# Performance work log

Hardware: AMD Instinct MI355X
Metric: run time of the kernel (lower is better)

## Reference

```python
import jax, jax.numpy as jnp
import numpy as np

B, T, D = 4, 2048, 1024
EPS = 1e-5


def _layernorm(x, g, b):
    mu = jnp.mean(x, axis=-1, keepdims=True)
    var = jnp.var(x, axis=-1, keepdims=True)
    return (x - mu) * jax.lax.rsqrt(var + EPS) * g + b


def setup_inputs() -> dict:
    key = jax.random.key(0)
    ks = jax.random.split(key, 16)
    s = lambda fan_in: 1.0 / np.sqrt(fan_in)
    return {
        "x": jax.random.normal(ks[0], (B, T, D), dtype=jnp.float32),
        "ln1_g": jnp.ones((D,), jnp.float32),
        "ln1_b": jnp.zeros((D,), jnp.float32),
        "Wqkv": jax.random.uniform(ks[1], (D, 3 * D), jnp.float32, -s(D), s(D)),
        "bqkv": jnp.zeros((3 * D,), jnp.float32),
        "Wproj": jax.random.uniform(ks[2], (D, D), jnp.float32, -s(D), s(D)),
        "bproj": jnp.zeros((D,), jnp.float32),
        "ln2_g": jnp.ones((D,), jnp.float32),
        "ln2_b": jnp.zeros((D,), jnp.float32),
        "W1": jax.random.uniform(ks[3], (D, 4 * D), jnp.float32, -s(D), s(D)),
        "b1": jnp.zeros((4 * D,), jnp.float32),
        "W2": jax.random.uniform(ks[4], (4 * D, D), jnp.float32, -s(4 * D), s(4 * D)),
        "b2": jnp.zeros((D,), jnp.float32),
    }


def reference(x, ln1_g, ln1_b, Wqkv, bqkv, Wproj, bproj, ln2_g, ln2_b, W1, b1, W2, b2):
    # NOTE: no residual connections in the original Block.
    h = _layernorm(x, ln1_g, ln1_b)
    kqv = h @ Wqkv + bqkv                      # [B,T,3D]
    k, q, v = jnp.split(kqv, 3, axis=-1)       # split order: k, q, v
    # Original scales by 1/sqrt(k.size(-1)) AFTER transposing k -> 1/sqrt(T).
    scores = jnp.einsum("btd,bsd->bts", q, k) * (1.0 / np.sqrt(T))
    causal = jnp.tril(jnp.ones((T, T), dtype=bool))
    scores = jnp.where(causal, scores, -jnp.inf)
    attn = jax.nn.softmax(scores, axis=-1)
    a = jnp.einsum("bts,bsd->btd", attn, v)
    a = a @ Wproj + bproj
    h2 = _layernorm(a, ln2_g, ln2_b)
    m = jax.nn.gelu(h2 @ W1 + b1, approximate=True)
    return m @ W2 + b2
```

## Files before the change

### kernel.cpp

```cpp
#include <hip/hip_runtime.h>
#include <hip/hip_bf16.h>

typedef __hip_bfloat16 bf16;
typedef __bf16 bf16x8 __attribute__((ext_vector_type(8)));
typedef __bf16 bf16x4 __attribute__((ext_vector_type(4)));
typedef __bf16 bf16x2 __attribute__((ext_vector_type(2)));
typedef float f32x4 __attribute__((ext_vector_type(4)));

static constexpr int Bq = 4, Tq = 2048, Dq = 1024;

__device__ inline float b2f(bf16 h) { return __bfloat162float(h); }
__device__ inline bf16 f2b(float f) { return __float2bfloat16(f); }

__device__ __forceinline__ void gload_lds16(const bf16* g, bf16* lds_wave_base) {
    __builtin_amdgcn_global_load_lds((const __attribute__((address_space(1))) void*)g,
                                     (__attribute__((address_space(3))) void*)lds_wave_base,
                                     16, 0, 0);
}

__device__ __forceinline__ float fast_gelu(float x) {
    float u = x * (0.7978845608028654f + 0.03567740814183427f * x * x);
    float e = __builtin_amdgcn_exp2f(-2.885390081777927f * u);
    return x * __builtin_amdgcn_rcpf(1.f + e);
}

__device__ inline void ld4f(const float* p, float* v) {
    float4 t = *reinterpret_cast<const float4*>(p);
    v[0] = t.x; v[1] = t.y; v[2] = t.z; v[3] = t.w;
}
__device__ inline void ld4f(const bf16* p, float* v) {
    bf16x4 t = *reinterpret_cast<const bf16x4*>(p);
    v[0] = (float)t[0]; v[1] = (float)t[1]; v[2] = (float)t[2]; v[3] = (float)t[3];
}

template <typename Tin>
__device__ __forceinline__ void ln_body(const Tin* __restrict__ x, const float* __restrict__ g,
                                        const float* __restrict__ b, bf16* __restrict__ out,
                                        int row, float* sred)
{
    const int tid = threadIdx.x;
    const int s0 = tid * 4;
    const Tin* xr = x + (size_t)row * Dq;
    bf16* orow = out + (size_t)row * Dq;
    float v[4], gv[4], bv[4];
    ld4f(xr + s0, v);
    ld4f(g + s0, gv);
    ld4f(b + s0, bv);
    float sum = v[0] + v[1] + v[2] + v[3];
    float sq = v[0]*v[0] + v[1]*v[1] + v[2]*v[2] + v[3]*v[3];
    for (int o = 32; o > 0; o >>= 1) { sum += __shfl_xor(sum, o); sq += __shfl_xor(sq, o); }
    const int w = tid >> 6;
    if ((tid & 63) == 0) { sred[w] = sum; sred[4 + w] = sq; }
    __syncthreads();
    const float ts = sred[0] + sred[1] + sred[2] + sred[3];
    const float tq = sred[4] + sred[5] + sred[6] + sred[7];
    const float mean = ts / Dq;
    const float rs = rsqrtf(tq / Dq - mean * mean + 1e-5f);
    bf16x4 o4;
    #pragma unroll
    for (int i = 0; i < 4; ++i) o4[i] = (__bf16)((v[i] - mean) * rs * gv[i] + bv[i]);
    *reinterpret_cast<bf16x4*>(orow + s0) = o4;
}

__global__ void ln_kernel(const bf16* __restrict__ x, const float* __restrict__ g,
                          const float* __restrict__ b, bf16* __restrict__ out)
{
    __shared__ float sred[8];
    ln_body(x, g, b, out, blockIdx.x, sred);
}

__global__ void prep_kernel(const float* __restrict__ x, const float* __restrict__ g,
                            const float* __restrict__ b, bf16* __restrict__ h,
                            const float* __restrict__ Wqkv, bf16* __restrict__ WqkvT,
                            const float* __restrict__ Wproj, bf16* __restrict__ WprojT,
                            const float* __restrict__ W1, bf16* __restrict__ W1T,
                            const float* __restrict__ W2, bf16* __restrict__ W2T)
{
    __shared__ float smem[64 * 65];
    int id = blockIdx.x;
    if (id < 8192) { ln_body(x, g, b, h, id, smem); return; }
    id -= 8192;
    const float* src; bf16* dst; long ldin, ldout; int gx;
    if (id < 768)       { src = Wqkv;  dst = WqkvT;  ldin = 3072; ldout = 1024; gx = 48; }
    else if (id < 1024) { id -= 768;  src = Wproj; dst = WprojT; ldin = 1024; ldout = 1024; gx = 16; }
    else if (id < 2048) { id -= 1024; src = W1;    dst = W1T;    ldin = 4096; ldout = 1024; gx = 64; }
    else                { id -= 2048; src = W2;    dst = W2T;    ldin = 1024; ldout = 4096; gx = 16; }
    const int c0 = (id % gx) * 64, r0 = (id / gx) * 64;
    const int tid = threadIdx.x;
    const int tx = tid & 63, ty = tid >> 6;
    float (*tile)[65] = reinterpret_cast<float(*)[65]>(smem);
    #pragma unroll
    for (int i = 0; i < 16; ++i) {
        int r = ty + i * 4;
        tile[r][tx] = src[(size_t)(r0 + r) * ldin + c0 + tx];
    }
    __syncthreads();
    const int px = tid & 31, cy = tid >> 5;
    #pragma unroll
    for (int i = 0; i < 8; ++i) {
        int cc = cy + i * 8;
        bf16x2 p;
        p[0] = (__bf16)tile[px * 2][cc];
        p[1] = (__bf16)tile[px * 2 + 1][cc];
        *reinterpret_cast<bf16x2*>(&dst[(size_t)(c0 + cc) * ldout + r0 + px * 2]) = p;
    }
}

template <int ACT, int TRI, int CK, int FR>
__global__ void gemm128(const bf16* __restrict__ A, const bf16* __restrict__ Bt,
                        const float* __restrict__ bias,
                        bf16* __restrict__ Cb, float* __restrict__ Cf,
                        int K, long lda, long ldb, long ldc,
                        long sA, long sB, long sC, float scale,
                        const bf16* __restrict__ vsrc, bf16* __restrict__ vdst)
{
    __shared__ bf16 As[128 * 64];
    __shared__ bf16 Bs[128 * 64];

    int bx, by;
    if (TRI) {
        const int lin = blockIdx.x;
        if (lin >= 136) {
            const int idx = lin - 136;
            const int c0 = (idx & 15) * 64, r0 = (idx >> 4) * 64;
            const bf16* ip = vsrc + (size_t)blockIdx.z * ((size_t)Tq * 3072);
            bf16* op = vdst + (size_t)blockIdx.z * ((size_t)Dq * Tq);
            bf16 (*tile)[66] = reinterpret_cast<bf16(*)[66]>(As);
            const int tid = threadIdx.x;
            const int tx = tid & 31, ty = tid >> 5;
            #pragma unroll
            for (int i = 0; i < 8; ++i) {
                int r = ty + i * 8;
                *reinterpret_cast<bf16x2*>(&tile[r][tx * 2]) =
                    *reinterpret_cast<const bf16x2*>(&ip[(size_t)(r0 + r) * 3072 + c0 + tx * 2]);
            }
            __syncthreads();
            #pragma unroll
            for (int i = 0; i < 8; ++i) {
                int cc = ty + i * 8;
                bf16x2 p;
                p[0] = tile[tx * 2][cc];
                p[1] = tile[tx * 2 + 1][cc];
                *reinterpret_cast<bf16x2*>(&op[(size_t)(c0 + cc) * 2048 + r0 + tx * 2]) = p;
            }
            return;
        }
        int t = (int)((sqrtf(8.f * lin + 1.f) - 1.f) * 0.5f);
        while ((t + 1) * (t + 2) / 2 <= lin) ++t;
        while (t * (t + 1) / 2 > lin) --t;
        by = t; bx = lin - t * (t + 1) / 2;
    } else {
        const int gx = gridDim.x, gy = gridDim.y;
        const int lin = blockIdx.x + gx * blockIdx.y;
        const int band = lin & 7;
        const int idx = lin >> 3;
        bx = idx % gx;
        by = band * (gy >> 3) + idx / gx;
    }

    const int m0 = by * 128, n0 = bx * 128;
    const int Kend = CK ? min(K, m0 + 128) : K;

    const bf16* Ab = A + (size_t)blockIdx.z * sA;
    const bf16* Bb = Bt + (size_t)blockIdx.z * sB;
    const int tid = threadIdx.x;
    const int wid = tid >> 6, lane = tid & 63;
    const int wr = wid >> 1, wc = wid & 1;
    const int l15 = lane & 15, quad = lane >> 4;

    const int rloc = lane >> 3, slot = lane & 7;
    const bf16* agp = Ab + (size_t)(m0 + wid * 32 + rloc) * lda + (slot ^ rloc) * 8;
    const bf16* bgp = Bb + (size_t)(n0 + wid * 32 + rloc) * ldb + (slot ^ rloc) * 8;
    bf16* awb = As + wid * 32 * 64;
    bf16* bwb = Bs + wid * 32 * 64;

    const int afo = (wr * 64 + l15) * 64 + ((quad ^ (l15 & 7)) * 8);
    const int bfo = (wc * 64 + l15) * 64 + ((quad ^ (l15 & 7)) * 8);

    f32x4 acc[4][4];
    #pragma unroll
    for (int i = 0; i < 4; ++i)
        #pragma unroll
        for (int j = 0; j < 4; ++j) acc[i][j] = (f32x4){0.f, 0.f, 0.f, 0.f};

    f32x4 acc_l[4];
    bf16x8 ones;
    if (FR) {
        #pragma unroll
        for (int i = 0; i < 4; ++i) acc_l[i] = (f32x4){0.f, 0.f, 0.f, 0.f};
        #pragma unroll
        for (int i = 0; i < 8; ++i) ones[i] = (__bf16)1.0f;
    }

    for (int k0 = 0; k0 < Kend; k0 += 64) {
        #pragma unroll
        for (int i = 0; i < 4; ++i) {
            gload_lds16(agp + k0 + (size_t)(i * 8) * lda, awb + i * 8 * 64);
            gload_lds16(bgp + k0 + (size_t)(i * 8) * ldb, bwb + i * 8 * 64);
        }
        __syncthreads();

        bf16x8 af0[4], bf0[4], af1[4], bf1[4];
        #pragma unroll
        for (int i = 0; i < 4; ++i) {
            af0[i] = *reinterpret_cast<const bf16x8*>(As + (afo ^ 0)  + i * 1024);
            af1[i] = *reinterpret_cast<const bf16x8*>(As + (afo ^ 32) + i * 1024);
        }
        #pragma unroll
        for (int j = 0; j < 4; ++j) {
            bf0[j] = *reinterpret_cast<const bf16x8*>(Bs + (bfo ^ 0)  + j * 1024);
            bf1[j] = *reinterpret_cast<const bf16x8*>(Bs + (bfo ^ 32) + j * 1024);
        }
        #pragma unroll
        for (int i = 0; i < 4; ++i)
            #pragma unroll
            for (int j = 0; j < 4; ++j)
                acc[i][j] = __builtin_amdgcn_mfma_f32_16x16x32_bf16(af0[i], bf0[j], acc[i][j], 0, 0, 0);
        if (FR) {
            #pragma unroll
            for (int i = 0; i < 4; ++i)
                acc_l[i] = __builtin_amdgcn_mfma_f32_16x16x32_bf16(af0[i], ones, acc_l[i], 0, 0, 0);
        }
        #pragma unroll
        for (int i = 0; i < 4; ++i)
            #pragma unroll
            for (int j = 0; j < 4; ++j)
                acc[i][j] = __builtin_amdgcn_mfma_f32_16x16x32_bf16(af1[i], bf1[j], acc[i][j], 0, 0, 0);
        if (FR) {
            #pragma unroll
            for (int i = 0; i < 4; ++i)
                acc_l[i] = __builtin_amdgcn_mfma_f32_16x16x32_bf16(af1[i], ones, acc_l[i], 0, 0, 0);
        }

        __syncthreads();
    }

    #pragma unroll
    for (int i = 0; i < 4; ++i) {
        const int row = m0 + wr * 64 + i * 16 + quad * 4;
        #pragma unroll
        for (int j = 0; j < 4; ++j) {
            const int col = n0 + wc * 64 + j * 16 + l15;
            const float bv = bias ? bias[col] : 0.f;
            #pragma unroll
            for (int r = 0; r < 4; ++r) {
                float vv = scale * acc[i][j][r] + bv;
                if (ACT == 1) vv = fast_gelu(vv);
                else if (ACT == 2)
                    vv = (col <= row + r) ? __builtin_amdgcn_exp2f(1.4426950408889634f * vv) : 0.f;
                if (FR) vv *= __builtin_amdgcn_rcpf(acc_l[i][r]);
                const size_t idx2 = (size_t)(row + r) * ldc + col + (size_t)blockIdx.z * sC;
                if (Cf) Cf[idx2] = vv;
                else    Cb[idx2] = f2b(vv);
            }
        }
    }
}

template <int ACT>
__global__ __launch_bounds__(512, 2) void gemm256(
        const bf16* __restrict__ A, const bf16* __restrict__ Bt,
        const float* __restrict__ bias, bf16* __restrict__ C,
        int K, long lda, long ldb, long ldc)
{
    __shared__ bf16 As[2][256 * 64];
    __shared__ bf16 Bs[2][256 * 64];

    const int gx = gridDim.x, gy = gridDim.y;
    const int lin = blockIdx.x + gx * blockIdx.y;
    const int band = lin & 7;
    const int idx = lin >> 3;
    const int bx = idx % gx;
    const int by = band * (gy >> 3) + idx / gx;
    const int m0 = by * 256, n0 = bx * 256;

    const int tid = threadIdx.x;
    const int wid = tid >> 6, lane = tid & 63;
    const int wr = wid >> 2, wc = wid & 3;
    const int l15 = lane & 15, quad = lane >> 4;
    const int rloc = lane >> 3, slot = lane & 7;

    const bf16* agp = A + (size_t)(m0 + wid * 8 + rloc) * lda + (slot ^ rloc) * 8;
    const bf16* bgp = Bt + (size_t)(n0 + wid * 8 + rloc) * ldb + (slot ^ rloc) * 8;

    auto issueA = [&](int buf, int t2, int R) {
        gload_lds16(agp + (size_t)R * lda + t2 * 64, &As[buf][(R + wid * 8) * 64]);
    };
    auto issueB = [&](int buf, int t2, int R) {
        gload_lds16(bgp + (size_t)R * ldb + t2 * 64, &Bs[buf][(R + wid * 8) * 64]);
    };

    const int xg = (quad ^ (l15 & 7)) * 8;
    const int afo = (wr * 128 + l15) * 64 + xg;
    const int bfo = (wc * 64 + l15) * 64 + xg;

    f32x4 acc[8][4];
    #pragma unroll
    for (int i = 0; i < 8; ++i)
        #pragma unroll
        for (int j = 0; j < 4; ++j) acc[i][j] = (f32x4){0.f, 0.f, 0.f, 0.f};

    const int nt = K >> 6;

    issueA(0, 0, 0); issueA(0, 0, 128);
    issueB(0, 0, 0); issueB(0, 0, 128); issueB(0, 0, 64); issueB(0, 0, 192);
    issueA(0, 0, 64); issueA(0, 0, 192);
    asm volatile("s_waitcnt vmcnt(2)" ::: "memory");
    __builtin_amdgcn_s_barrier();

#define PH_READS(p, rh, ks)                                                              \
    {   const int xr = (ks) << 5;                                                        \
        _Pragma("unroll")                                                                \
        for (int i = 0; i < 4; ++i)                                                      \
            a[i] = *reinterpret_cast<const bf16x8*>(&As[p][(afo + ((rh)*4 + i) * 1024) ^ xr]); \
        _Pragma("unroll")                                                                \
        for (int j = 0; j < 4; ++j)                                                      \
            b[j] = *reinterpret_cast<const bf16x8*>(&Bs[p][(bfo + (j) * 1024) ^ xr]);    \
    }
#define PH_MFMA(rh)                                                                      \
    {   __builtin_amdgcn_s_setprio(1);                                                   \
        _Pragma("unroll")                                                                \
        for (int i = 0; i < 4; ++i)                                                      \
            _Pragma("unroll")                                                            \
            for (int j = 0; j < 4; ++j)                                                  \
                acc[(rh)*4 + i][j] =                                                     \
                    __builtin_amdgcn_mfma_f32_16x16x32_bf16(a[i], b[j], acc[(rh)*4 + i][j], 0, 0, 0); \
        __builtin_amdgcn_s_setprio(0);                                                   \
    }
#define BAR()   __builtin_amdgcn_s_barrier()
#define LGKM0() asm volatile("s_waitcnt lgkmcnt(0)" ::: "memory")

    for (int t = 0; t < nt; ++t) {
        const int p = t & 1, q = p ^ 1, tn = t + 1;
        const bool pre = tn < nt;
        bf16x8 a[4], b[4];

        PH_READS(p, 0, 0);
        if (pre) { issueA(q, tn, 0); issueA(q, tn, 128); issueB(q, tn, 0); }
        BAR(); LGKM0();
        PH_MFMA(0);
        BAR();

        PH_READS(p, 0, 1);
        if (pre) { issueB(q, tn, 128); issueB(q, tn, 64); issueB(q, tn, 192); }
        BAR(); LGKM0();
        PH_MFMA(0);
        if (pre) asm volatile("s_waitcnt vmcnt(6)" ::: "memory");
        else     asm volatile("s_waitcnt vmcnt(0)" ::: "memory");
        BAR();

        PH_READS(p, 1, 0);
        BAR(); LGKM0();
        PH_MFMA(1);
        BAR();

        PH_READS(p, 1, 1);
        if (pre) { issueA(q, tn, 64); issueA(q, tn, 192); }
        BAR(); LGKM0();
        PH_MFMA(1);
        if (pre) asm volatile("s_waitcnt vmcnt(2)" ::: "memory");
        else     asm volatile("s_waitcnt vmcnt(0)" ::: "memory");
        BAR();
    }
#undef PH_READS
#undef PH_MFMA
#undef BAR
#undef LGKM0

    #pragma unroll
    for (int i = 0; i < 8; ++i) {
        const int row = m0 + wr * 128 + i * 16 + quad * 4;
        #pragma unroll
        for (int j = 0; j < 4; ++j) {
            const int col = n0 + wc * 64 + j * 16 + l15;
            const float bv = bias ? bias[col] : 0.f;
            #pragma unroll
            for (int r = 0; r < 4; ++r) {
                float vv = acc[i][j][r] + bv;
                if (ACT == 1) vv = fast_gelu(vv);
                C[(size_t)(row + r) * ldc + col] = f2b(vv);
            }
        }
    }
}

extern "C" void kernel_launch(void* const* d_in, const int* in_sizes, int n_in,
                              void* d_out, int out_size, void* d_ws, size_t ws_size,
                              hipStream_t stream)
{
    (void)in_sizes; (void)n_in; (void)out_size; (void)ws_size;
    const float* x     = (const float*)d_in[0];
    const float* ln1g  = (const float*)d_in[1];
    const float* ln1b  = (const float*)d_in[2];
    const float* Wqkv  = (const float*)d_in[3];
    const float* bqkv  = (const float*)d_in[4];
    const float* Wproj = (const float*)d_in[5];
    const float* bproj = (const float*)d_in[6];
    const float* ln2g  = (const float*)d_in[7];
    const float* ln2b  = (const float*)d_in[8];
    const float* W1    = (const float*)d_in[9];
    const float* b1    = (const float*)d_in[10];
    const float* W2    = (const float*)d_in[11];
    const float* b2    = (const float*)d_in[12];
    float* out = (float*)d_out;

    char* ws = (char*)d_ws;
    size_t off = 0;
    auto alloc = [&](size_t elems) { bf16* p = (bf16*)(ws + off); off += elems * sizeof(bf16); return p; };
    bf16* WqkvT  = alloc(3072UL * 1024);
    bf16* WprojT = alloc(1024UL * 1024);
    bf16* W1T    = alloc(4096UL * 1024);
    bf16* W2T    = alloc(1024UL * 4096);
    bf16* h      = alloc(8192UL * 1024);
    bf16* kqv    = alloc(8192UL * 3072);
    bf16* vT     = alloc(4UL * 1024 * 2048);
    bf16* attn   = alloc(4UL * 2048 * 2048);
    bf16* a   = h;
    bf16* p   = kqv;
    bf16* h2  = kqv + 8192UL * 1024;
    bf16* m   = kqv + 2UL * 8192 * 1024;

    const long T3D = (long)Tq * 3072, TT = (long)Tq * Tq, DT = (long)Dq * Tq, TD = (long)Tq * Dq;

    prep_kernel<<<11264, 256, 0, stream>>>(x, ln1g, ln1b, h,
                                           Wqkv, WqkvT, Wproj, WprojT, W1, W1T, W2, W2T);

    gemm256<0><<<dim3(12, 32, 1), 512, 0, stream>>>(h, WqkvT, bqkv, kqv,
        1024, 1024L, 1024L, 3072L);

    gemm128<2,1,0,0><<<dim3(648, 1, 4), 256, 0, stream>>>(kqv + 1024, kqv, nullptr, attn, nullptr,
        1024, 3072L, 3072L, 2048L, T3D, T3D, TT, 0.022097086912079608f, kqv + 2048, vT);

    gemm128<0,0,1,1><<<dim3(8, 16, 4), 256, 0, stream>>>(attn, vT, nullptr, a, nullptr,
        2048, 2048L, 2048L, 1024L, TT, DT, TD, 1.f, nullptr, nullptr);

    gemm128<0,0,0,0><<<dim3(8, 64, 1), 256, 0, stream>>>(a, WprojT, bproj, p, nullptr,
        1024, 1024L, 1024L, 1024L, 0L, 0L, 0L, 1.f, nullptr, nullptr);

    ln_kernel<<<8192, 256, 0, stream>>>(p, ln2g, ln2b, h2);

    gemm256<1><<<dim3(16, 32, 1), 512, 0, stream>>>(h2, W1T, b1, m,
        1024, 1024L, 1024L, 4096L);

    gemm128<0,0,0,0><<<dim3(8, 64, 1), 256, 0, stream>>>(m, W2T, b2, nullptr, out,
        4096, 4096L, 4096L, 1024L, 0L, 0L, 0L, 1.f, nullptr, nullptr);
}
```

Measured before the change: 493.3 us.

## Software-pipeline LDS fragment reads with double register sets across GEMM phases

Restructures the GEMM main loop so LDS fragment reads for the next phase are issued before the current phase's MFMAs, using two register sets (ax/ay, b0r/btr) and partial lgkmcnt waits instead of waiting for zero each time. The loop is unrolled by two tiles with fixed buffer indices, and the first fragments of the next tile are prefetched at the end of each tile. This is meant to hide LDS read latency behind matrix-core work, at the cost of more registers and a trickier barrier/wait schedule. It also assumes the tile count is even and removes some B-fragment rereads.

```diff
diff --git a/kernel.cpp b/kernel.cpp
--- a/kernel.cpp
+++ b/kernel.cpp
@@ -300,72 +300,86 @@
         #pragma unroll
         for (int j = 0; j < 4; ++j) acc[i][j] = (f32x4){0.f, 0.f, 0.f, 0.f};
 
+    bf16x8 ax[4], ay[4], b0r[4], btr[4];
+
     const int nt = K >> 6;
 
+#define RD_A(buf, rh, ks, dst)                                                            \
+    { _Pragma("unroll")                                                                   \
+      for (int i_ = 0; i_ < 4; ++i_)                                                      \
+          dst[i_] = *reinterpret_cast<const bf16x8*>(                                     \
+              &As[buf][(afo + (rh) * 4096 + i_ * 1024) ^ ((ks) * 32)]); }
+#define RD_B(buf, ks, dst)                                                                \
+    { _Pragma("unroll")                                                                   \
+      for (int j_ = 0; j_ < 4; ++j_)                                                      \
+          dst[j_] = *reinterpret_cast<const bf16x8*>(                                     \
+              &Bs[buf][(bfo + j_ * 1024) ^ ((ks) * 32)]); }
+#define MF(rh, Aset, Bset)                                                                \
+    { __builtin_amdgcn_s_setprio(1);                                                      \
+      _Pragma("unroll")                                                                   \
+      for (int i_ = 0; i_ < 4; ++i_)                                                      \
+          _Pragma("unroll")                                                               \
+          for (int j_ = 0; j_ < 4; ++j_)                                                  \
+              acc[(rh) * 4 + i_][j_] = __builtin_amdgcn_mfma_f32_16x16x32_bf16(           \
+                  Aset[i_], Bset[j_], acc[(rh) * 4 + i_][j_], 0, 0, 0);                   \
+      __builtin_amdgcn_s_setprio(0); }
+#define BAR()    __builtin_amdgcn_s_barrier()
+#define CFENCE() asm volatile("" ::: "memory")
+#define LGKM(n)  asm volatile("s_waitcnt lgkmcnt(" #n ")" ::: "memory")
+
     issueA(0, 0, 0); issueA(0, 0, 128);
-    issueB(0, 0, 0); issueB(0, 0, 128); issueB(0, 0, 64); issueB(0, 0, 192);
+    issueB(0, 0, 0); issueB(0, 0, 64); issueB(0, 0, 128); issueB(0, 0, 192);
     issueA(0, 0, 64); issueA(0, 0, 192);
     asm volatile("s_waitcnt vmcnt(2)" ::: "memory");
-    __builtin_amdgcn_s_barrier();
-
-#define PH_READS(p, rh, ks)                                                              \
-    {   const int xr = (ks) << 5;                                                        \
-        _Pragma("unroll")                                                                \
-        for (int i = 0; i < 4; ++i)                                                      \
-            a[i] = *reinterpret_cast<const bf16x8*>(&As[p][(afo + ((rh)*4 + i) * 1024) ^ xr]); \
-        _Pragma("unroll")                                                                \
-        for (int j = 0; j < 4; ++j)                                                      \
-            b[j] = *reinterpret_cast<const bf16x8*>(&Bs[p][(bfo + (j) * 1024) ^ xr]);    \
-    }
-#define PH_MFMA(rh)                                                                      \
-    {   __builtin_amdgcn_s_setprio(1);                                                   \
-        _Pragma("unroll")                                                                \
-        for (int i = 0; i < 4; ++i)                                                      \
-            _Pragma("unroll")                                                            \
-            for (int j = 0; j < 4; ++j)                                                  \
-                acc[(rh)*4 + i][j] =                                                     \
-                    __builtin_amdgcn_mfma_f32_16x16x32_bf16(a[i], b[j], acc[(rh)*4 + i][j], 0, 0, 0); \
-        __builtin_amdgcn_s_setprio(0);                                                   \
-    }
-#define BAR()   __builtin_amdgcn_s_barrier()
-#define LGKM0() asm volatile("s_waitcnt lgkmcnt(0)" ::: "memory")
-
-    for (int t = 0; t < nt; ++t) {
-        const int p = t & 1, q = p ^ 1, tn = t + 1;
-        const bool pre = tn < nt;
-        bf16x8 a[4], b[4];
-
-        PH_READS(p, 0, 0);
-        if (pre) { issueA(q, tn, 0); issueA(q, tn, 128); issueB(q, tn, 0); }
-        BAR(); LGKM0();
-        PH_MFMA(0);
-        BAR();
-
-        PH_READS(p, 0, 1);
-        if (pre) { issueB(q, tn, 128); issueB(q, tn, 64); issueB(q, tn, 192); }
-        BAR(); LGKM0();
-        PH_MFMA(0);
-        if (pre) asm volatile("s_waitcnt vmcnt(6)" ::: "memory");
-        else     asm volatile("s_waitcnt vmcnt(0)" ::: "memory");
-        BAR();
-
-        PH_READS(p, 1, 0);
-        BAR(); LGKM0();
-        PH_MFMA(1);
-        BAR();
-
-        PH_READS(p, 1, 1);
-        if (pre) { issueA(q, tn, 64); issueA(q, tn, 192); }
-        BAR(); LGKM0();
-        PH_MFMA(1);
-        if (pre) asm volatile("s_waitcnt vmcnt(2)" ::: "memory");
-        else     asm volatile("s_waitcnt vmcnt(0)" ::: "memory");
-        BAR();
-    }
-#undef PH_READS
-#undef PH_MFMA
+    BAR(); CFENCE();
+    RD_A(0, 0, 0, ax);
+    RD_B(0, 0, b0r);
+
+#define TILE_BODY(bufp, bufq, tn, PRE)                                                    \
+                           \
+    if (PRE) { issueA(bufq, tn, 0); issueA(bufq, tn, 128);                                \
+               issueB(bufq, tn, 0); issueB(bufq, tn, 64); }                               \
+    RD_A(bufp, 0, 1, ay); RD_B(bufp, 1, btr);                                             \
+    BAR();                                                                                \
+    LGKM(8);                                                                              \
+    MF(0, ax, b0r);                                                                       \
+    if (PRE) asm volatile("s_waitcnt vmcnt(4)" ::: "memory");                             \
+    else     asm volatile("s_waitcnt vmcnt(0)" ::: "memory");                             \
+    BAR(); CFENCE();                                                                      \
+                         \
+    if (PRE) { issueB(bufq, tn, 128); issueB(bufq, tn, 192); }                            \
+    RD_A(bufp, 1, 0, ax);                                                                 \
+    BAR();                                                                                \
+    LGKM(4);                                                                              \
+    MF(0, ay, btr);                                                                       \
+    BAR();                                                                                \
+                           \
+    if (PRE) { issueA(bufq, tn, 64); issueA(bufq, tn, 192); }                             \
+    RD_A(bufp, 1, 1, ay); RD_B(bufp, 1, btr);                                             \
+    BAR();                                                                                \
+    LGKM(8);                                                                              \
+    MF(1, ax, b0r);                                                                       \
+    BAR();                                                                                \
+               \
+    LGKM(0);                                                                              \
+    MF(1, ay, btr);                                                                       \
+    if (PRE) asm volatile("s_waitcnt vmcnt(2)" ::: "memory");                             \
+    else     asm volatile("s_waitcnt vmcnt(0)" ::: "memory");                             \
+    BAR(); CFENCE();                                                                      \
+    if (PRE) { RD_A(bufq, 0, 0, ax); RD_B(bufq, 0, b0r); }
+
+    for (int t = 0; t < nt; t += 2) {
+        TILE_BODY(0, 1, t + 1, true);
+        const bool pre2 = (t + 2) < nt;
+        TILE_BODY(1, 0, t + 2, pre2);
+    }
+#undef TILE_BODY
+#undef RD_A
+#undef RD_B
+#undef MF
 #undef BAR
-#undef LGKM0
+#undef CFENCE
+#undef LGKM
 
     #pragma unroll
     for (int i = 0; i < 8; ++i) {
```

After: 545.7 us. 10.6% more time.
